# Performance work log

Hardware: AMD Instinct MI355X
Metric: run time of the kernel (lower is better)

Reference implementation:

```python
import jax, jax.numpy as jnp
import numpy as np

ALPHA_MIN = 0.08
ALPHA_MAX = 0.45
BETA = 0.12
SIG_SLOPE = 8.0
SIG_OFFSET = 1.5
EPS = 1e-12


def setup_inputs() -> dict:
    key = jax.random.key(0)
    k1, k2, k3 = jax.random.split(key, 3)
    B, F, T = 8, 64, 2048
    phases = jax.random.normal(k1, (B, F, T), dtype=jnp.float32) * jnp.float32(np.pi)
    prev_coh = jax.random.uniform(k2, (B,), dtype=jnp.float32)  # coherence in [0,1)
    # previous alpha lives in [alpha_min, alpha_max]
    prev_alpha = ALPHA_MIN + (ALPHA_MAX - ALPHA_MIN) * jax.random.uniform(k3, (B,), dtype=jnp.float32)
    return {"phases": phases, "prev_coh": prev_coh, "prev_alpha": prev_alpha}


def reference(phases, prev_coh, prev_alpha):
    phases = phases.astype(jnp.float32)
    # phase-locking value per channel: |mean_t exp(i*phase)|  -> [B, F]
    plv = jnp.abs(jnp.mean(jnp.exp(1j * phases), axis=-1))
    # pairwise phase differences: diff[b,f,g,t] = phases[b,f,t] - phases[b,g,t]
    diff = phases[..., :, None, :] - phases[..., None, :, :]          # [B, F, F, T]
    triad = diff + jnp.swapaxes(diff, -2, -3)                          # [B, F, F, T] (identically 0)
    triad_mag = jnp.abs(jnp.mean(jnp.exp(1j * triad), axis=-1))        # [B, F, F]
    diag = jnp.diagonal(triad_mag, axis1=-2, axis2=-1)                 # [B, F]
    coh = jnp.clip(jnp.mean(jnp.sqrt(plv * diag + EPS), axis=-1), 0.0, 1.0)  # [B]
    # sigmoid hysteresis EMA update (non-empty-state branch)
    velocity = coh - prev_coh
    target_alpha = ALPHA_MIN + (ALPHA_MAX - ALPHA_MIN) * jax.nn.sigmoid(
        SIG_SLOPE * jnp.abs(velocity) - SIG_OFFSET)
    alpha = prev_alpha + BETA * (target_alpha - prev_alpha)            # lerp(prev, target, beta)
    smoothed = alpha * coh + (1.0 - alpha) * prev_coh
    return smoothed
```

## Files before the change

### kernel.cpp

```cpp
#include <hip/hip_runtime.h>
#include <math.h>

#define FCH 64
#define TLEN 2048

__global__ __launch_bounds__(256) void plv_kernel(
    const float* __restrict__ phases, float* __restrict__ ws) {
    const int bf  = blockIdx.x;
    const int tid = threadIdx.x;
    const float4* p = (const float4*)(phases + (size_t)bf * TLEN);

    float cs = 0.0f, ss = 0.0f;
#pragma unroll
    for (int i = 0; i < 2; ++i) {
        float4 v = p[i * 256 + tid];
        float s, c;
        sincosf(v.x, &s, &c); cs += c; ss += s;
        sincosf(v.y, &s, &c); cs += c; ss += s;
        sincosf(v.z, &s, &c); cs += c; ss += s;
        sincosf(v.w, &s, &c); cs += c; ss += s;
    }

#pragma unroll
    for (int off = 32; off > 0; off >>= 1) {
        cs += __shfl_down(cs, off);
        ss += __shfl_down(ss, off);
    }
    __shared__ float scs[4], sss[4];
    const int wave = tid >> 6;
    if ((tid & 63) == 0) { scs[wave] = cs; sss[wave] = ss; }
    __syncthreads();
    if (tid == 0) {
        float c = scs[0] + scs[1] + scs[2] + scs[3];
        float s = sss[0] + sss[1] + sss[2] + sss[3];
        float plv = sqrtf(c * c + s * s) * (1.0f / (float)TLEN);
        ws[bf] = sqrtf(plv + 1e-12f);
    }
}

__global__ __launch_bounds__(512) void finish_kernel(
    const float* __restrict__ ws,
    const float* __restrict__ prev_coh,
    const float* __restrict__ prev_alpha,
    float* __restrict__ out, int B) {
    const int tid = threadIdx.x;
    const int b = tid >> 6;
    float s = (b < B) ? ws[tid] : 0.0f;
#pragma unroll
    for (int off = 32; off > 0; off >>= 1) s += __shfl_down(s, off);
    if ((tid & 63) == 0 && b < B) {
        float coh = s * (1.0f / (float)FCH);
        coh = fminf(fmaxf(coh, 0.0f), 1.0f);
        float pc = prev_coh[b];
        float v = coh - pc;
        float x = 8.0f * fabsf(v) - 1.5f;
        float sig = 1.0f / (1.0f + expf(-x));
        float target = 0.08f + (0.45f - 0.08f) * sig;
        float pa = prev_alpha[b];
        float alpha = pa + 0.12f * (target - pa);
        out[b] = alpha * coh + (1.0f - alpha) * pc;
    }
}

extern "C" void kernel_launch(void* const* d_in, const int* in_sizes, int n_in,
                              void* d_out, int out_size, void* d_ws, size_t ws_size,
                              hipStream_t stream) {
    const float* phases     = (const float*)d_in[0];
    const float* prev_coh   = (const float*)d_in[1];
    const float* prev_alpha = (const float*)d_in[2];
    float* out = (float*)d_out;
    float* ws  = (float*)d_ws;

    const int B = in_sizes[1];
    const int n_bf = B * FCH;

    plv_kernel<<<n_bf, 256, 0, stream>>>(phases, ws);
    finish_kernel<<<1, n_bf, 0, stream>>>(ws, prev_coh, prev_alpha, out, B);
}
```

Before: 60.22 us.

## Fuse PLV and finish kernels into one block per batch

Replaces the two-kernel pipeline (one block per batch-channel row, then a single-block finish kernel) with one kernel that launches one 1024-thread block per batch. Each of the block's waves handles four channels, writes its per-channel value to shared memory, and the first wave runs the final reduction and the EMA update. This removes the second launch and the workspace round trip through global memory. In exchange the grid shrinks from 512 blocks to 8, so only a handful of compute units share the sincos-heavy work.

```diff
diff --git a/kernel.cpp b/kernel.cpp
--- a/kernel.cpp
+++ b/kernel.cpp
@@ -4,61 +4,64 @@
 #define FCH 64
 #define TLEN 2048
 
-__global__ __launch_bounds__(256) void plv_kernel(
-    const float* __restrict__ phases, float* __restrict__ ws) {
-    const int bf  = blockIdx.x;
-    const int tid = threadIdx.x;
-    const float4* p = (const float4*)(phases + (size_t)bf * TLEN);
+__global__ __launch_bounds__(1024) void fused_kernel(
+    const float* __restrict__ phases,
+    const float* __restrict__ prev_coh,
+    const float* __restrict__ prev_alpha,
+    float* __restrict__ out) {
+    const int b    = blockIdx.x;
+    const int tid  = threadIdx.x;
+    const int wave = tid >> 6;
+    const int lane = tid & 63;
 
-    float cs = 0.0f, ss = 0.0f;
-#pragma unroll
-    for (int i = 0; i < 2; ++i) {
-        float4 v = p[i * 256 + tid];
-        float s, c;
-        sincosf(v.x, &s, &c); cs += c; ss += s;
-        sincosf(v.y, &s, &c); cs += c; ss += s;
-        sincosf(v.z, &s, &c); cs += c; ss += s;
-        sincosf(v.w, &s, &c); cs += c; ss += s;
-    }
+    __shared__ float svals[FCH];
+
+    const float4* base = (const float4*)(phases + (size_t)b * FCH * TLEN);
 
 #pragma unroll
-    for (int off = 32; off > 0; off >>= 1) {
-        cs += __shfl_down(cs, off);
-        ss += __shfl_down(ss, off);
+    for (int c = 0; c < 4; ++c) {
+        const int f = (wave << 2) | c;
+        const float4* p = base + (size_t)f * (TLEN / 4);
+
+        float cs = 0.0f, ss = 0.0f;
+#pragma unroll
+        for (int i = 0; i < 8; ++i) {
+            float4 v = p[i * 64 + lane];
+            float s, cth;
+            sincosf(v.x, &s, &cth); cs += cth; ss += s;
+            sincosf(v.y, &s, &cth); cs += cth; ss += s;
+            sincosf(v.z, &s, &cth); cs += cth; ss += s;
+            sincosf(v.w, &s, &cth); cs += cth; ss += s;
+        }
+
+#pragma unroll
+        for (int off = 32; off > 0; off >>= 1) {
+            cs += __shfl_down(cs, off);
+            ss += __shfl_down(ss, off);
+        }
+        if (lane == 0) {
+            float plv = sqrtf(cs * cs + ss * ss) * (1.0f / (float)TLEN);
+            svals[f] = sqrtf(plv + 1e-12f);
+        }
     }
-    __shared__ float scs[4], sss[4];
-    const int wave = tid >> 6;
-    if ((tid & 63) == 0) { scs[wave] = cs; sss[wave] = ss; }
     __syncthreads();
-    if (tid == 0) {
-        float c = scs[0] + scs[1] + scs[2] + scs[3];
-        float s = sss[0] + sss[1] + sss[2] + sss[3];
-        float plv = sqrtf(c * c + s * s) * (1.0f / (float)TLEN);
-        ws[bf] = sqrtf(plv + 1e-12f);
-    }
-}
 
-__global__ __launch_bounds__(512) void finish_kernel(
-    const float* __restrict__ ws,
-    const float* __restrict__ prev_coh,
-    const float* __restrict__ prev_alpha,
-    float* __restrict__ out, int B) {
-    const int tid = threadIdx.x;
-    const int b = tid >> 6;
-    float s = (b < B) ? ws[tid] : 0.0f;
+    if (wave == 0) {
+        float s = svals[lane];
 #pragma unroll
-    for (int off = 32; off > 0; off >>= 1) s += __shfl_down(s, off);
-    if ((tid & 63) == 0 && b < B) {
-        float coh = s * (1.0f / (float)FCH);
-        coh = fminf(fmaxf(coh, 0.0f), 1.0f);
-        float pc = prev_coh[b];
-        float v = coh - pc;
-        float x = 8.0f * fabsf(v) - 1.5f;
-        float sig = 1.0f / (1.0f + expf(-x));
-        float target = 0.08f + (0.45f - 0.08f) * sig;
-        float pa = prev_alpha[b];
-        float alpha = pa + 0.12f * (target - pa);
-        out[b] = alpha * coh + (1.0f - alpha) * pc;
+        for (int off = 32; off > 0; off >>= 1) s += __shfl_down(s, off);
+        if (lane == 0) {
+            float coh = s * (1.0f / (float)FCH);
+            coh = fminf(fmaxf(coh, 0.0f), 1.0f);
+            float pc  = prev_coh[b];
+            float v   = coh - pc;
+            float x   = 8.0f * fabsf(v) - 1.5f;
+            float sig = 1.0f / (1.0f + expf(-x));
+            float target = 0.08f + (0.45f - 0.08f) * sig;
+            float pa = prev_alpha[b];
+            float alpha = pa + 0.12f * (target - pa);
+            out[b] = alpha * coh + (1.0f - alpha) * pc;
+        }
     }
 }
 
@@ -69,11 +72,9 @@
     const float* prev_coh   = (const float*)d_in[1];
     const float* prev_alpha = (const float*)d_in[2];
     float* out = (float*)d_out;
-    float* ws  = (float*)d_ws;
+    (void)d_ws; (void)ws_size;
 
     const int B = in_sizes[1];
-    const int n_bf = B * FCH;
 
-    plv_kernel<<<n_bf, 256, 0, stream>>>(phases, ws);
-    finish_kernel<<<1, n_bf, 0, stream>>>(ws, prev_coh, prev_alpha, out, B);
+    fused_kernel<<<B, 1024, 0, stream>>>(phases, prev_coh, prev_alpha, out);
 }
```

Result: slower. 100.2 us (+66.4%).
